# Kernel optimization log

Measured on AMD Instinct MI355X. Metric: run time of the kernel, lower is better.

The kernel has to match this reference:

```python
import math
import jax, jax.numpy as jnp
import numpy as np

WQ = (24, 24)  # query window size
WK = (12, 12)  # key window size
NH = 8         # heads
D = 256        # d_model


def _ln(x, g, b, eps=1e-5):
    m = x.mean(-1, keepdims=True)
    v = ((x - m) ** 2).mean(-1, keepdims=True)
    return (x - m) / jnp.sqrt(v + eps) * g + b


def _sine_pos(F, Hp, Wp):
    # Faithful to PositionEmbeddingSine(normalize=True) applied to an NHWC tensor:
    # dim F (grid height) plays the role of channels; returns (F, Hp, Wp).
    npf = F // 2
    scale = 2.0 * math.pi
    eps = 1e-5
    y = jnp.arange(1, Hp + 1, dtype=jnp.float32) / (Hp + eps) * scale
    x = jnp.arange(1, Wp + 1, dtype=jnp.float32) / (Wp + eps) * scale
    dim_t = 10000.0 ** (2.0 * (jnp.arange(npf) // 2).astype(jnp.float32) / npf)
    def enc(e):
        p = e[:, None] / dim_t
        return jnp.stack([jnp.sin(p[:, 0::2]), jnp.cos(p[:, 1::2])], axis=2).reshape(e.shape[0], npf)
    py = enc(y)  # (Hp, npf)
    px = enc(x)  # (Wp, npf)
    pos = jnp.concatenate([
        jnp.broadcast_to(py[:, None, :], (Hp, Wp, npf)),
        jnp.broadcast_to(px[None, :, :], (Hp, Wp, npf))], axis=-1)
    return pos.transpose(2, 0, 1)


def _interp_ac(x, Ho, Wo):
    # bilinear, align_corners=True; x: (B, C, H, W)
    B, C, H, W = x.shape
    ys = jnp.linspace(0.0, H - 1.0, Ho)
    xs = jnp.linspace(0.0, W - 1.0, Wo)
    y0 = jnp.floor(ys).astype(jnp.int32); y1 = jnp.minimum(y0 + 1, H - 1); wy = ys - y0
    x0 = jnp.floor(xs).astype(jnp.int32); x1 = jnp.minimum(x0 + 1, W - 1); wx = xs - x0
    rows = x[:, :, y0, :] * (1 - wy)[None, None, :, None] + x[:, :, y1, :] * wy[None, None, :, None]
    return rows[:, :, :, x0] * (1 - wx) + rows[:, :, :, x1] * wx


def _wpart(x, wh, ww):
    B, H, W, C = x.shape
    return x.reshape(B, H // wh, wh, W // ww, ww, C).transpose(0, 1, 3, 2, 4, 5).reshape(-1, wh * ww, C)


def _avgpool(x, wh, ww):
    B, H, W, C = x.shape
    return x.reshape(B, H // wh, wh, W // ww, ww, C).mean(axis=(2, 4))


def _forward(x1, x2, q_w, q_b, k_w, k_b, v_w, v_b, q2_w, q2_b, k2_w, k2_b, v2_w, v2_b,
             proj_w, proj_b, proj_g, proj_beta, n1_g, n1_b, n2_g, n2_b,
             fc1_w, fc1_b, fc2_w, fc2_b):
    B, C1, H1, W1 = x1.shape
    _, C2, H2, W2 = x2.shape
    hd = D // NH
    x1n = x1.transpose(0, 2, 3, 1)
    sc = _ln(x1n @ proj_w + proj_b, proj_g, proj_beta)
    sc = _interp_ac(sc.transpose(0, 3, 1, 2), H2, W2).transpose(0, 2, 3, 1)
    x1p = jnp.pad(x1n, ((0, 0), (0, (-H1) % WK[0]), (0, (-W1) % WK[1]), (0, 0)))
    x2n = x2.transpose(0, 2, 3, 1)
    x2p = jnp.pad(x2n, ((0, 0), (0, (-H2) % WQ[0]), (0, (-W2) % WQ[1]), (0, 0)))
    H2p, W2p = x2p.shape[1], x2p.shape[2]
    qw = _wpart(x2p, *WQ)  # (B*nw, 576, C2)
    kw = _wpart(x1p, *WK)  # (B*nw, 144, C1)
    Bn, N1, _ = qw.shape
    def heads(t):
        return t.reshape(t.shape[0], t.shape[1], NH, hd).transpose(0, 2, 1, 3)
    q = heads(qw @ q_w + q_b)
    k = heads(kw @ k_w + k_b)
    v = heads(kw @ v_w + v_b)
    # NOTE: faithful to the source: scale = head_dim**(-0.0) == 1.0 and NO softmax here
    attn = q @ k.transpose(0, 1, 3, 2)
    o = (attn @ v).transpose(0, 2, 1, 3).reshape(Bn, N1, D)
    nwh, nww = H2p // WQ[0], W2p // WQ[1]
    o = o.reshape(B, nwh, nww, WQ[0], WQ[1], D).transpose(0, 1, 3, 2, 4, 5).reshape(B, H2p, W2p, D)
    qf = x2p + o
    # global (pooled) cross-attention branch
    qg = _avgpool(x2p, *WQ)
    qg = qg + _sine_pos(qg.shape[1], qg.shape[2], qg.shape[3])[None]
    kg = _avgpool(x1p, *WK)
    kg = kg + _sine_pos(kg.shape[1], kg.shape[2], kg.shape[3])[None]
    qg = qg.reshape(B, -1, C2)
    kg = kg.reshape(B, -1, C1)
    Nw = qg.shape[1]
    qg2 = heads(qg @ q2_w + q2_b)
    kg2 = heads(kg @ k2_w + k2_b)
    vg = heads(kg @ v2_w + v2_b)
    a2 = jax.nn.softmax(qg2 @ kg2.transpose(0, 1, 3, 2), axis=-1)
    og = (a2 @ vg).transpose(0, 2, 1, 3).reshape(B, Nw, D)
    og = og.transpose(0, 2, 1).reshape(B, D, nwh, nww)
    og = _interp_ac(og, H2p, W2p).transpose(0, 2, 3, 1)
    qf = (qf + og)[:, :H2, :W2, :]
    h = _ln(qf, n1_g, n1_b)
    h = jax.nn.gelu(h @ fc1_w + fc1_b, approximate=False) @ fc2_w + fc2_b
    out = sc + h
    return _ln(out, n2_g, n2_b).transpose(0, 3, 1, 2)


def setup_inputs() -> dict:
    key = jax.random.key(0)
    ks = jax.random.split(key, 12)
    B, C1, C2 = 2, 512, 256
    H1, W1, H2, W2 = 96, 96, 192, 192
    s = 0.02
    def lin(k, i, o):
        return jax.random.normal(k, (i, o), jnp.float32) * s
    return {
        'x1': jax.random.normal(ks[0], (B, C1, H1, W1), jnp.float32),
        'x2': jax.random.normal(ks[1], (B, C2, H2, W2), jnp.float32),
        'q_w': lin(ks[2], C2, D), 'q_b': jnp.zeros((D,), jnp.float32),
        'k_w': lin(ks[3], C1, D), 'k_b': jnp.zeros((D,), jnp.float32),
        'v_w': lin(ks[4], C1, D), 'v_b': jnp.zeros((D,), jnp.float32),
        'q2_w': lin(ks[5], C2, D), 'q2_b': jnp.zeros((D,), jnp.float32),
        'k2_w': lin(ks[6], C1, D), 'k2_b': jnp.zeros((D,), jnp.float32),
        'v2_w': lin(ks[7], C1, D), 'v2_b': jnp.zeros((D,), jnp.float32),
        'proj_w': lin(ks[8], C1, D), 'proj_b': jnp.zeros((D,), jnp.float32),
        'proj_g': jnp.ones((D,), jnp.float32), 'proj_beta': jnp.zeros((D,), jnp.float32),
        'n1_g': jnp.ones((D,), jnp.float32), 'n1_b': jnp.zeros((D,), jnp.float32),
        'n2_g': jnp.ones((D,), jnp.float32), 'n2_b': jnp.zeros((D,), jnp.float32),
        'fc1_w': lin(ks[9], D, 2 * D), 'fc1_b': jnp.zeros((2 * D,), jnp.float32),
        'fc2_w': lin(ks[10], 2 * D, D), 'fc2_b': jnp.zeros((D,), jnp.float32),
    }


def reference(x1, x2, q_w, q_b, k_w, k_b, v_w, v_b, q2_w, q2_b, k2_w, k2_b, v2_w, v2_b,
              proj_w, proj_b, proj_g, proj_beta, n1_g, n1_b, n2_g, n2_b,
              fc1_w, fc1_b, fc2_w, fc2_b):
    return _forward(x1, x2, q_w, q_b, k_w, k_b, v_w, v_b, q2_w, q2_b, k2_w, k2_b, v2_w, v2_b,
                    proj_w, proj_b, proj_g, proj_beta, n1_g, n1_b, n2_g, n2_b,
                    fc1_w, fc1_b, fc2_w, fc2_b)
```

## Files before the change

kernel.cpp:

```cpp
#include <hip/hip_runtime.h>
#include <math.h>


#define HW1 9216L
#define HW2 36864L
#define M1  18432L
#define M2  73728L

typedef __attribute__((ext_vector_type(8))) short short8;
typedef __attribute__((ext_vector_type(4))) float f32x4;
typedef unsigned short u16;

__device__ __forceinline__ short f2bf(float f)
{
    unsigned u = __builtin_bit_cast(unsigned, f);
    u = (u + 0x7fff + ((u >> 16) & 1)) >> 16;
    return (short)u;
}
__device__ __forceinline__ float bf2f(u16 u)
{
    unsigned x = ((unsigned)u) << 16;
    return __builtin_bit_cast(float, x);
}
__device__ __forceinline__ float gelu_exact(float v)
{
    return 0.5f * v * (1.0f + erff(v * 0.70710678118654752f));
}

__global__ __launch_bounds__(256) void wcvt(
    const float* __restrict__ pw, const float* __restrict__ kw,
    const float* __restrict__ vw, const float* __restrict__ qw,
    const float* __restrict__ f1, const float* __restrict__ f2,
    u16* __restrict__ pwT, u16* __restrict__ kwT, u16* __restrict__ vwT,
    u16* __restrict__ qwT, u16* __restrict__ f1T, u16* __restrict__ f2T)
{
    int bx = blockIdx.x, t = threadIdx.x;
    const float* src; u16* dst; int K, ldN = 256, kt, n0 = 0;
    if (bx < 32)       { src = pw; dst = pwT; K = 512; kt = bx; }
    else if (bx < 64)  { src = kw; dst = kwT; K = 512; kt = bx - 32; }
    else if (bx < 96)  { src = vw; dst = vwT; K = 512; kt = bx - 64; }
    else if (bx < 112) { src = qw; dst = qwT; K = 256; kt = bx - 96; }
    else if (bx < 144) { int j = bx - 112; src = f1; dst = f1T; K = 256;
                         ldN = 512; kt = j >> 1; n0 = (j & 1) * 256; }
    else               { src = f2; dst = f2T; K = 512; kt = bx - 144; }
    int n = n0 + t, k0 = kt * 16;
    short s[16];
#pragma unroll
    for (int kk = 0; kk < 16; ++kk) s[kk] = f2bf(src[(long)(k0 + kk) * ldN + n]);
    *(short8*)&dst[(long)n * K + k0]     = *(short8*)&s[0];
    *(short8*)&dst[(long)n * K + k0 + 8] = *(short8*)&s[8];
}

__device__ __forceinline__ float pe4(int t, float e)
{
    if (t == 0) return sinf(e);
    if (t == 1) return cosf(e);
    if (t == 2) return sinf(e * 0.01f);
    return cosf(e * 0.01f);
}

__global__ __launch_bounds__(256) void x1t(
    const float* __restrict__ x1, u16* __restrict__ x1bf, float* __restrict__ kg)
{
    __shared__ short T[6144];
    __shared__ float rw[64][8];
    const int blk = blockIdx.x;
    const int b = blk / 768, rem = blk % 768;
    const int cg = rem / 96, y = rem % 96;
    const int t = threadIdx.x;

    ((float2*)rw)[t] = float2{0.f, 0.f};
    __syncthreads();

    const float* src = x1 + ((long)(b * 512 + cg * 64)) * HW1 + (long)y * 96;
#pragma unroll
    for (int k = 0; k < 6; ++k) {
        int idx = t + k * 256;
        int c = idx / 24, col4 = idx % 24;
        float4 v = *(const float4*)(src + (long)c * HW1 + col4 * 4);
        atomicAdd(&rw[c][col4 / 3], v.x + v.y + v.z + v.w);
        int chh = c >> 1, cb = c & 1;
        const float* vf = (const float*)&v;
#pragma unroll
        for (int j = 0; j < 4; ++j) {
            int pix = col4 * 4 + j;
            int word = pix * 32 + (chh ^ (((pix >> 2) & 7) << 2));
            T[word * 2 + cb] = f2bf(vf[j]);
        }
    }
    __syncthreads();
    u16* dst = x1bf + ((long)b * HW1 + (long)y * 96) * 512 + cg * 64;
#pragma unroll
    for (int k = 0; k < 3; ++k) {
        int idx = t + k * 256;
        int pix = idx >> 3, j = idx & 7;
        int w0 = pix * 32 + ((j * 4) ^ (((pix >> 2) & 7) << 2));
        *(short8*)(dst + (long)pix * 512 + j * 8) = *(short8*)&T[w0 * 2];
    }

    {
        int wy = y / 12;
#pragma unroll
        for (int u = 0; u < 2; ++u) {
            int cell = t * 2 + u;
            int c = cell >> 3, wx = cell & 7;
            atomicAdd(kg + (long)(b * 64 + wy * 8 + wx) * 512 + cg * 64 + c,
                      rw[c][wx] * (1.0f / 144.0f));
        }
    }
    if (y % 12 == 0) {
        const float TWO_PI = 6.283185307179586f;
        int wy = y / 12;
#pragma unroll
        for (int u = 0; u < 2; ++u) {
            int cell = t * 2 + u;
            int gxx = cell & 7, c = cg * 64 + (cell >> 3);
            float pos;
            if (wy < 4) pos = pe4(wy,     (gxx + 1) * (TWO_PI / (8.0f + 1e-5f)));
            else        pos = pe4(wy - 4, (c + 1)   * (TWO_PI / (512.0f + 1e-5f)));
            atomicAdd(kg + (long)(b * 64 + wy * 8 + gxx) * 512 + c, pos);
        }
    }
}

__global__ __launch_bounds__(256) void x2t(
    const float* __restrict__ x2, u16* __restrict__ x2pm, float* __restrict__ qg)
{
    __shared__ short T[12288];
    __shared__ float qsum[64][8];
    const int blk = blockIdx.x;
    const int b = blk / 768, rem = blk % 768;
    const int cg = rem / 192, h = rem % 192;
    const int t = threadIdx.x;

    ((float2*)qsum)[t] = float2{0.f, 0.f};
    __syncthreads();

    const float* src = x2 + ((long)(b * 256 + cg * 64) * 192 + h) * 192;
#pragma unroll
    for (int k = 0; k < 12; ++k) {
        int idx = t + k * 256;
        int c = idx / 48, col4 = idx % 48;
        float4 v = *(const float4*)(src + (long)c * HW2 + col4 * 4);
        atomicAdd(&qsum[c][col4 / 6], v.x + v.y + v.z + v.w);
        int chh = c >> 1, cb = c & 1;
        const float* vf = (const float*)&v;
#pragma unroll
        for (int j = 0; j < 4; ++j) {
            int pix = col4 * 4 + j;
            int word = pix * 32 + (chh ^ (((pix >> 2) & 7) << 2));
            T[word * 2 + cb] = f2bf(vf[j]);
        }
    }
    __syncthreads();

    u16* dst = x2pm + ((long)b * HW2 + (long)h * 192) * 256 + cg * 64;
#pragma unroll
    for (int k = 0; k < 6; ++k) {
        int idx = t + k * 256;
        int pix = idx >> 3, j = idx & 7;
        int w0 = pix * 32 + ((j * 4) ^ (((pix >> 2) & 7) << 2));
        *(short8*)(dst + (long)pix * 256 + j * 8) = *(short8*)&T[w0 * 2];
    }

    {
        int wy = h / 24;
#pragma unroll
        for (int u = 0; u < 2; ++u) {
            int cell = t * 2 + u;
            int c = cell >> 3, wx = cell & 7;
            atomicAdd(qg + (long)(b * 64 + wy * 8 + wx) * 256 + cg * 64 + c,
                      qsum[c][wx] * (1.0f / 576.0f));
        }
    }
    if (h % 24 == 0) {
        const float TWO_PI = 6.283185307179586f;
        int wy = h / 24;
#pragma unroll
        for (int u = 0; u < 2; ++u) {
            int cell = t * 2 + u;
            int gxx = cell & 7, c = cg * 64 + (cell >> 3);
            float pos;
            if (wy < 4) pos = pe4(wy,     (gxx + 1) * (TWO_PI / (8.0f + 1e-5f)));
            else        pos = pe4(wy - 4, (c + 1)   * (TWO_PI / (256.0f + 1e-5f)));
            atomicAdd(qg + (long)(b * 64 + wy * 8 + gxx) * 256 + c, pos);
        }
    }
}

__global__ __launch_bounds__(256) void proj_ln(
    const u16* __restrict__ A, const u16* __restrict__ BT,
    const float* __restrict__ bias, const float* __restrict__ g,
    const float* __restrict__ beta, u16* __restrict__ Cout)
{
    __shared__ short pool[64 * 72 + 256 * 72];
    short* As = pool;
    short* Bs = pool + 64 * 72;
    const int t = threadIdx.x;
    const long m0 = (long)blockIdx.x * 64;
    const int w = t >> 6, lane = t & 63;
    const int lm = lane & 15, lq = lane >> 4;

    f32x4 acc[16] = {};
    for (int k0 = 0; k0 < 512; k0 += 64) {
#pragma unroll
        for (int it = 0; it < 2; ++it) {
            int idx = t + it * 256;
            int r = idx >> 3, q = idx & 7;
            *(short8*)&As[r * 72 + q * 8] = *(const short8*)(A + (m0 + r) * 512 + k0 + q * 8);
        }
#pragma unroll
        for (int it = 0; it < 8; ++it) {
            int idx = t + it * 256;
            int n = idx >> 3, q = idx & 7;
            *(short8*)&Bs[n * 72 + q * 8] = *(const short8*)(BT + (long)n * 512 + k0 + q * 8);
        }
        __syncthreads();
#pragma unroll
        for (int kk = 0; kk < 64; kk += 32) {
            short8 af = *(short8*)&As[(w * 16 + lm) * 72 + kk + lq * 8];
#pragma unroll
            for (int c = 0; c < 16; ++c) {
                short8 bf = *(short8*)&Bs[(c * 16 + lm) * 72 + kk + lq * 8];
                acc[c] = __builtin_amdgcn_mfma_f32_16x16x32_bf16(af, bf, acc[c], 0, 0, 0);
            }
        }
        __syncthreads();
    }
#pragma unroll
    for (int c = 0; c < 16; ++c) {
        float bv = bias[c * 16 + lm];
#pragma unroll
        for (int i = 0; i < 4; ++i) acc[c][i] += bv;
    }
    short* ob = pool;
#pragma unroll
    for (int i = 0; i < 4; ++i) {
        float s = 0.f, s2 = 0.f;
#pragma unroll
        for (int c = 0; c < 16; ++c) { float v = acc[c][i]; s += v; s2 += v * v; }
#pragma unroll
        for (int o = 8; o > 0; o >>= 1) {
            s  += __shfl_xor(s,  o, 64);
            s2 += __shfl_xor(s2, o, 64);
        }
        float mean = s * (1.0f / 256.0f);
        float var  = s2 * (1.0f / 256.0f) - mean * mean;
        float rs   = rsqrtf(var + 1e-5f);
        int row = w * 16 + lq * 4 + i;
#pragma unroll
        for (int c = 0; c < 16; ++c) {
            int col = c * 16 + lm;
            ob[row * 264 + col] = f2bf((acc[c][i] - mean) * rs * g[col] + beta[col]);
        }
    }
    __syncthreads();
    {
        int sr = t >> 2, q4 = (t & 3) * 64;
        u16* Cp = Cout + (m0 + sr) * 256 + q4;
#pragma unroll
        for (int q = 0; q < 8; ++q)
            *(short8*)(Cp + q * 8) = *(short8*)&ob[sr * 264 + q4 + q * 8];
    }
}

template<int EPI>
__global__ __launch_bounds__(256) void gemm_lds(
    const u16* __restrict__ A, const u16* __restrict__ BT,
    const float* __restrict__ bias, u16* __restrict__ C,
    int N, int K, int ldA)
{
    __shared__ short pool[18432];
    short* As = pool;
    short* Bs = pool + 128 * 72;
    const int tid = threadIdx.x;
    const int m0 = blockIdx.y * 128;
    const int n0 = blockIdx.x * 128;
    const int w = tid >> 6, lane = tid & 63;
    const int wm = (w & 1) * 64, wn = (w >> 1) * 64;
    const int lm = lane & 15, lq = lane >> 4;

    const int sr = tid >> 1, sh = (tid & 1) * 32;
    const u16* Ap = A  + (long)(m0 + sr) * ldA + sh;
    const u16* Bp = BT + (long)(n0 + sr) * K   + sh;

    f32x4 acc[4][4] = {};

    for (int k0 = 0; k0 < K; k0 += 64) {
#pragma unroll
        for (int q = 0; q < 4; ++q)
            *(short8*)&As[sr * 72 + sh + q * 8] = *(const short8*)(Ap + k0 + q * 8);
#pragma unroll
        for (int q = 0; q < 4; ++q)
            *(short8*)&Bs[sr * 72 + sh + q * 8] = *(const short8*)(Bp + k0 + q * 8);
        __syncthreads();
#pragma unroll
        for (int kk = 0; kk < 64; kk += 32) {
            short8 af[4], bfr[4];
#pragma unroll
            for (int r = 0; r < 4; ++r) af[r]  = *(short8*)&As[(wm + r * 16 + lm) * 72 + kk + lq * 8];
#pragma unroll
            for (int c = 0; c < 4; ++c) bfr[c] = *(short8*)&Bs[(wn + c * 16 + lm) * 72 + kk + lq * 8];
#pragma unroll
            for (int r = 0; r < 4; ++r)
#pragma unroll
                for (int c = 0; c < 4; ++c)
                    acc[r][c] = __builtin_amdgcn_mfma_f32_16x16x32_bf16(af[r], bfr[c], acc[r][c], 0, 0, 0);
        }
        __syncthreads();
    }

    short* ob = pool;
#pragma unroll
    for (int r = 0; r < 4; ++r)
#pragma unroll
        for (int i = 0; i < 4; ++i) {
            int row = wm + r * 16 + lq * 4 + i;
#pragma unroll
            for (int c = 0; c < 4; ++c) {
                int jl = wn + c * 16 + lm;
                float v = acc[r][c][i] + bias[n0 + jl];
                if (EPI == 1) v = gelu_exact(v);
                ob[row * 136 + jl] = f2bf(v);
            }
        }
    __syncthreads();
    int m = tid >> 1, half = (tid & 1) * 64;
    u16* Cp = C + (long)(m0 + m) * N + n0 + half;
#pragma unroll
    for (int q = 0; q < 8; ++q)
        *(short8*)(Cp + q * 8) = *(short8*)&ob[m * 136 + half + q * 8];
}

__global__ __launch_bounds__(256) void wattn_ln2(
    const u16* __restrict__ x2pm, const u16* __restrict__ qwbT,
    const float* __restrict__ qbias, const u16* __restrict__ ktvb,
    const float* __restrict__ og, u16* __restrict__ hln,
    const float* __restrict__ n1g, const float* __restrict__ n1b)
{
    __shared__ short qs[48 * 288];

    const int t = threadIdx.x;
    const int blk = blockIdx.x;
    const int strip = blk % 12, win = blk / 12;
    const int b = win >> 6, wy = (win >> 3) & 7, wxw = win & 7;
    const int hh0 = wy * 24 + strip * 2;
    const int w = t >> 6, lane = t & 63;
    const int lm = lane & 15, lq = lane >> 4;

    long pbase[3];
#pragma unroll
    for (int r = 0; r < 3; ++r) {
        int p = r * 16 + lm;
        pbase[r] = ((long)b * HW2 + (long)(hh0 + p / 24) * 192 + wxw * 24 + (p % 24)) * 256;
    }

    f32x4 acc[3][4] = {};
#pragma unroll 2
    for (int kc = 0; kc < 8; ++kc) {
        const int ko = kc * 32 + lq * 8;
        short8 af[3], bfr[4];
#pragma unroll
        for (int r = 0; r < 3; ++r)
            af[r] = *(const short8*)(x2pm + pbase[r] + ko);
#pragma unroll
        for (int c = 0; c < 4; ++c)
            bfr[c] = *(const short8*)(qwbT + (long)(w * 64 + c * 16 + lm) * 256 + ko);
#pragma unroll
        for (int r = 0; r < 3; ++r)
#pragma unroll
            for (int c = 0; c < 4; ++c)
                acc[r][c] = __builtin_amdgcn_mfma_f32_16x16x32_bf16(af[r], bfr[c], acc[r][c], 0, 0, 0);
    }

#pragma unroll
    for (int c = 0; c < 4; ++c) {
        float bv = qbias[w * 64 + c * 16 + lm];
#pragma unroll
        for (int r = 0; r < 3; ++r)
#pragma unroll
            for (int i = 0; i < 4; ++i) {
                int row = r * 16 + lq * 4 + i;
                int col = w * 64 + c * 16 + lm;
                qs[row * 288 + (col ^ (((row >> 2) & 3) << 3))] = f2bf(acc[r][c][i] + bv);
            }
    }

    f32x4 oacc[2][3][2] = {};
#pragma unroll
    for (int hl = 0; hl < 2; ++hl) {
        int h = w * 2 + hl;
        short8 af2[3], bfr2[2];
#pragma unroll
        for (int r = 0; r < 3; ++r) {
            int row = r * 16 + lm;
            af2[r] = *(short8*)&qs[row * 288 + ((h * 32 + lq * 8) ^ (((row >> 2) & 3) << 3))];
        }
#pragma unroll
        for (int c = 0; c < 2; ++c)
            bfr2[c] = *(const short8*)(ktvb + ((long)(win * 8 + h) * 32 + c * 16 + lm) * 32 + lq * 8);
#pragma unroll
        for (int r = 0; r < 3; ++r)
#pragma unroll
            for (int c = 0; c < 2; ++c)
                oacc[hl][r][c] = __builtin_amdgcn_mfma_f32_16x16x32_bf16(af2[r], bfr2[c], oacc[hl][r][c], 0, 0, 0);
    }

#pragma unroll
    for (int hl = 0; hl < 2; ++hl)
#pragma unroll
        for (int c = 0; c < 2; ++c)
#pragma unroll
            for (int r = 0; r < 3; ++r)
#pragma unroll
                for (int i = 0; i < 4; ++i) {
                    int p = r * 16 + lq * 4 + i;
                    int ch = (w * 2 + hl) * 32 + c * 16 + lm;
                    qs[p * 288 + (ch ^ (((p >> 2) & 3) << 3))] = f2bf(oacc[hl][r][c][i]);
                }
    __syncthreads();

    float4 g4 = *(const float4*)(n1g + lane * 4);
    float4 b4 = *(const float4*)(n1b + lane * 4);
    const float* ogb0 = og + (long)b * 64 * 256;
#pragma unroll
    for (int pp = 0; pp < 12; ++pp) {
        int p = w * 12 + pp;
        int hh = hh0 + (p / 24), ww = wxw * 24 + (p % 24);
        float fy = hh * (7.0f / 191.0f);
        int y0 = (int)fy; int y1 = min(y0 + 1, 7); float wyf = fy - y0;
        float fx = ww * (7.0f / 191.0f);
        int x0 = (int)fx; int x1 = min(x0 + 1, 7); float wxf = fx - x0;
        float w00 = (1.f - wyf) * (1.f - wxf), w01 = (1.f - wyf) * wxf;
        float w10 = wyf * (1.f - wxf),         w11 = wyf * wxf;
        float4 q00 = *(const float4*)(ogb0 + (y0 * 8 + x0) * 256 + lane * 4);
        float4 q01 = *(const float4*)(ogb0 + (y0 * 8 + x1) * 256 + lane * 4);
        float4 q10 = *(const float4*)(ogb0 + (y1 * 8 + x0) * 256 + lane * 4);
        float4 q11 = *(const float4*)(ogb0 + (y1 * 8 + x1) * 256 + lane * 4);
        long pix = (long)b * HW2 + (long)hh * 192 + ww;
        ushort4 rv = *(const ushort4*)(x2pm + pix * 256 + lane * 4);
        int sw = ((p >> 2) & 3) << 3;
        ushort4 ov = *(ushort4*)&qs[p * 288 + ((lane * 4) ^ sw)];
        float xv0 = bf2f(rv.x) + bf2f(ov.x) + (w00 * q00.x + w01 * q01.x + w10 * q10.x + w11 * q11.x);
        float xv1 = bf2f(rv.y) + bf2f(ov.y) + (w00 * q00.y + w01 * q01.y + w10 * q10.y + w11 * q11.y);
        float xv2 = bf2f(rv.z) + bf2f(ov.z) + (w00 * q00.z + w01 * q01.z + w10 * q10.z + w11 * q11.z);
        float xv3 = bf2f(rv.w) + bf2f(ov.w) + (w00 * q00.w + w01 * q01.w + w10 * q10.w + w11 * q11.w);
        float s  = xv0 + xv1 + xv2 + xv3;
        float s2 = xv0 * xv0 + xv1 * xv1 + xv2 * xv2 + xv3 * xv3;
#pragma unroll
        for (int o = 32; o > 0; o >>= 1) {
            s  += __shfl_xor(s,  o, 64);
            s2 += __shfl_xor(s2, o, 64);
        }
        float mean = s * (1.0f / 256.0f);
        float var  = s2 * (1.0f / 256.0f) - mean * mean;
        float rs   = rsqrtf(var + 1e-5f);
        ushort4 o4;
        o4.x = (u16)f2bf((xv0 - mean) * rs * g4.x + b4.x);
        o4.y = (u16)f2bf((xv1 - mean) * rs * g4.y + b4.y);
        o4.z = (u16)f2bf((xv2 - mean) * rs * g4.z + b4.z);
        o4.w = (u16)f2bf((xv3 - mean) * rs * g4.w + b4.w);
        *(ushort4*)(hln + pix * 256 + lane * 4) = o4;
    }
}

__global__ __launch_bounds__(64) void ktv_mfma(
    const u16* __restrict__ kb, const u16* __restrict__ vb, u16* __restrict__ ktvb)
{
    __shared__ short kt[32 * 162];
    __shared__ short vt[32 * 162];
    const int blk = blockIdx.x;
    const int win = blk >> 3, hd = blk & 7;
    const int b = win >> 6, wy = (win >> 3) & 7, wx = win & 7;
    const int t = threadIdx.x;
    const int lm = t & 15, lq = t >> 4;

    {
        int c = t >> 1, p0 = 144 + (t & 1) * 8;
#pragma unroll
        for (int j = 0; j < 8; ++j) {
            kt[c * 162 + p0 + j] = 0;
            vt[c * 162 + p0 + j] = 0;
        }
    }
    const int pq = t >> 2, c8 = (t & 3) * 8;
#pragma unroll
    for (int it = 0; it < 9; ++it) {
        int p = it * 16 + pq;
        int py = p / 12, px = p % 12;
        long m = (long)b * HW1 + (long)(wy * 12 + py) * 96 + wx * 12 + px;
        short8 kvk = *(const short8*)(kb + m * 256 + hd * 32 + c8);
        short8 kvv = *(const short8*)(vb + m * 256 + hd * 32 + c8);
#pragma unroll
        for (int j = 0; j < 8; ++j) {
            kt[(c8 + j) * 162 + p] = kvk[j];
            vt[(c8 + j) * 162 + p] = kvv[j];
        }
    }
    __syncthreads();
    f32x4 acc[2][2] = {};
#pragma unroll
    for (int kk = 0; kk < 160; kk += 32) {
        short8 af[2], bf[2];
#pragma unroll
        for (int r = 0; r < 2; ++r) af[r] = *(short8*)&kt[(r * 16 + lm) * 162 + kk + lq * 8];
#pragma unroll
        for (int c = 0; c < 2; ++c) bf[c] = *(short8*)&vt[(c * 16 + lm) * 162 + kk + lq * 8];
#pragma unroll
        for (int r = 0; r < 2; ++r)
#pragma unroll
            for (int c = 0; c < 2; ++c)
                acc[r][c] = __builtin_amdgcn_mfma_f32_16x16x32_bf16(af[r], bf[c], acc[r][c], 0, 0, 0);
    }
    u16* dst = ktvb + (long)blk * 1024;
#pragma unroll
    for (int r = 0; r < 2; ++r)
#pragma unroll
        for (int c = 0; c < 2; ++c)
#pragma unroll
            for (int i = 0; i < 4; ++i)
                dst[(c * 16 + lm) * 32 + r * 16 + lq * 4 + i] = (u16)f2bf(acc[r][c][i]);
}

__global__ __launch_bounds__(256) void gemm64m(
    const float* __restrict__ qg, const float* __restrict__ kg,
    const float* __restrict__ q2w, const float* __restrict__ q2b,
    const float* __restrict__ k2w, const float* __restrict__ k2b,
    const float* __restrict__ v2w, const float* __restrict__ v2b,
    float* __restrict__ qg2, float* __restrict__ kg2, float* __restrict__ vgb)
{
    const float* A; const float* Bm; const float* bias; float* C; int K, ldA;
    int z = blockIdx.z;
    if (z == 0)      { A = qg; Bm = q2w; bias = q2b; C = qg2; K = 256; ldA = 256; }
    else if (z == 1) { A = kg; Bm = k2w; bias = k2b; C = kg2; K = 512; ldA = 512; }
    else             { A = kg; Bm = v2w; bias = v2b; C = vgb; K = 512; ldA = 512; }
    const int N = 256;
    constexpr int BK = 16;
    __shared__ float As[BK][68];
    __shared__ float Bs[BK][68];
    const int tid = threadIdx.x;
    const int m0 = blockIdx.y * 64;
    const int n0 = blockIdx.x * 64;
    const int tm = (tid >> 4) << 2;
    const int tn = (tid & 15) << 2;
    float acc[4][4] = {};
    for (int k0 = 0; k0 < K; k0 += BK) {
#pragma unroll
        for (int it = 0; it < 4; ++it) {
            int idx = tid + it * 256;
            int my = idx >> 4, kx = idx & 15;
            As[kx][my] = A[(long)(m0 + my) * ldA + (k0 + kx)];
        }
#pragma unroll
        for (int it = 0; it < 4; ++it) {
            int idx = tid + it * 256;
            int ky = idx >> 6, nx = idx & 63;
            Bs[ky][nx] = Bm[(long)(k0 + ky) * N + (n0 + nx)];
        }
        __syncthreads();
#pragma unroll
        for (int kk = 0; kk < BK; ++kk) {
            float a[4], b[4];
#pragma unroll
            for (int i = 0; i < 4; ++i) a[i] = As[kk][tm + i];
#pragma unroll
            for (int j = 0; j < 4; ++j) b[j] = Bs[kk][tn + j];
#pragma unroll
            for (int i = 0; i < 4; ++i)
#pragma unroll
                for (int j = 0; j < 4; ++j) acc[i][j] += a[i] * b[j];
        }
        __syncthreads();
    }
#pragma unroll
    for (int i = 0; i < 4; ++i) {
        long row = (long)(m0 + tm + i) * N;
#pragma unroll
        for (int j = 0; j < 4; ++j)
            C[row + n0 + tn + j] = acc[i][j] + bias[n0 + tn + j];
    }
}

__global__ __launch_bounds__(256) void gattn(
    const float* __restrict__ qg2, const float* __restrict__ kg2,
    const float* __restrict__ vg, float* __restrict__ og)
{
    __shared__ float qh[64][33], kh[64][33], vh[64][33];
    __shared__ float S[64][65];
    __shared__ float rinv[64];
    int blk = blockIdx.x;
    int b = blk >> 3, hd = blk & 7;
    int t = threadIdx.x;
#pragma unroll
    for (int it = 0; it < 8; ++it) {
        int idx = t + it * 256;
        int n = idx >> 5, i = idx & 31;
        long src = (long)(b * 64 + n) * 256 + hd * 32 + i;
        qh[n][i] = qg2[src];
        kh[n][i] = kg2[src];
        vh[n][i] = vg[src];
    }
    __syncthreads();
    int r = t >> 2, qq = t & 3, c0 = qq * 16;
    for (int c = c0; c < c0 + 16; ++c) {
        float s = 0.f;
#pragma unroll
        for (int i = 0; i < 32; ++i) s += qh[r][i] * kh[c][i];
        S[r][c] = s;
    }
    __syncthreads();
    float mx = -1e30f;
    for (int c = c0; c < c0 + 16; ++c) mx = fmaxf(mx, S[r][c]);
    mx = fmaxf(mx, __shfl_xor(mx, 1, 64));
    mx = fmaxf(mx, __shfl_xor(mx, 2, 64));
    float sm = 0.f;
    for (int c = c0; c < c0 + 16; ++c) {
        float e = expf(S[r][c] - mx);
        S[r][c] = e;
        sm += e;
    }
    sm += __shfl_xor(sm, 1, 64);
    sm += __shfl_xor(sm, 2, 64);
    if (qq == 0) rinv[r] = 1.0f / sm;
    __syncthreads();
    int n = t >> 2, j0 = (t & 3) * 8;
    float inv = rinv[n];
    for (int j = j0; j < j0 + 8; ++j) {
        float s = 0.f;
        for (int c = 0; c < 64; ++c) s += S[n][c] * vh[c][j];
        og[(long)(b * 64 + n) * 256 + hd * 32 + j] = s * inv;
    }
}

__global__ __launch_bounds__(256) void final_k3(
    const u16* __restrict__ mlp, const u16* __restrict__ sc,
    const float* __restrict__ g, const float* __restrict__ bb,
    float* __restrict__ out)
{
    __shared__ float lnb[32][258];
    int blk = blockIdx.x;
    int b = blk / 1152;
    int rem = blk - b * 1152;
    int hh = rem / 6, ww0 = (rem % 6) * 32;
    int wv = threadIdx.x >> 6, lane = threadIdx.x & 63;
    int c0 = lane * 4;
    float4 g4 = *(const float4*)(g + c0);
    float4 b4 = *(const float4*)(bb + c0);
    float fy = hh * (95.0f / 191.0f);
    int y0 = (int)fy; int y1 = min(y0 + 1, 95); float wy = fy - y0;
    const u16* scb = sc + (long)b * 9216 * 256 + c0;
#pragma unroll
    for (int i = 0; i < 8; ++i) {
        int p = wv * 8 + i;
        int ww = ww0 + p;
        float fx = ww * (95.0f / 191.0f);
        int x0 = (int)fx; int x1 = min(x0 + 1, 95); float wx = fx - x0;
        ushort4 u00 = *(const ushort4*)(scb + (long)(y0 * 96 + x0) * 256);
        ushort4 u01 = *(const ushort4*)(scb + (long)(y0 * 96 + x1) * 256);
        ushort4 u10 = *(const ushort4*)(scb + (long)(y1 * 96 + x0) * 256);
        ushort4 u11 = *(const ushort4*)(scb + (long)(y1 * 96 + x1) * 256);
        long m = ((long)b * 192 + hh) * 192 + ww;
        ushort4 um = *(const ushort4*)(mlp + m * 256 + c0);
        float w00 = (1.f - wy) * (1.f - wx), w01 = (1.f - wy) * wx;
        float w10 = wy * (1.f - wx),         w11 = wy * wx;
        float xv0 = bf2f(um.x) + w00 * bf2f(u00.x) + w01 * bf2f(u01.x) + w10 * bf2f(u10.x) + w11 * bf2f(u11.x);
        float xv1 = bf2f(um.y) + w00 * bf2f(u00.y) + w01 * bf2f(u01.y) + w10 * bf2f(u10.y) + w11 * bf2f(u11.y);
        float xv2 = bf2f(um.z) + w00 * bf2f(u00.z) + w01 * bf2f(u01.z) + w10 * bf2f(u10.z) + w11 * bf2f(u11.z);
        float xv3 = bf2f(um.w) + w00 * bf2f(u00.w) + w01 * bf2f(u01.w) + w10 * bf2f(u10.w) + w11 * bf2f(u11.w);
        float s  = xv0 + xv1 + xv2 + xv3;
        float s2 = xv0 * xv0 + xv1 * xv1 + xv2 * xv2 + xv3 * xv3;
#pragma unroll
        for (int o = 32; o > 0; o >>= 1) {
            s  += __shfl_xor(s,  o, 64);
            s2 += __shfl_xor(s2, o, 64);
        }
        float mean = s * (1.0f / 256.0f);
        float var  = s2 * (1.0f / 256.0f) - mean * mean;
        float rs   = rsqrtf(var + 1e-5f);
        lnb[p][c0 + 0] = (xv0 - mean) * rs * g4.x + b4.x;
        lnb[p][c0 + 1] = (xv1 - mean) * rs * g4.y + b4.y;
        lnb[p][c0 + 2] = (xv2 - mean) * rs * g4.z + b4.z;
        lnb[p][c0 + 3] = (xv3 - mean) * rs * g4.w + b4.w;
    }
    __syncthreads();
    int tw = threadIdx.x & 31, cg = threadIdx.x >> 5;
#pragma unroll
    for (int cc = 0; cc < 32; ++cc) {
        int c = cg * 32 + cc;
        out[((long)(b * 256 + c) * 192 + hh) * 192 + ww0 + tw] = lnb[tw][c];
    }
}

extern "C" void kernel_launch(void* const* d_in, const int* in_sizes, int n_in,
                              void* d_out, int out_size, void* d_ws, size_t ws_size,
                              hipStream_t stream)
{
    const float* x1     = (const float*)d_in[0];
    const float* x2     = (const float*)d_in[1];
    const float* q_w    = (const float*)d_in[2];
    const float* q_b    = (const float*)d_in[3];
    const float* k_w    = (const float*)d_in[4];
    const float* k_b    = (const float*)d_in[5];
    const float* v_w    = (const float*)d_in[6];
    const float* v_b    = (const float*)d_in[7];
    const float* q2_w   = (const float*)d_in[8];
    const float* q2_b   = (const float*)d_in[9];
    const float* k2_w   = (const float*)d_in[10];
    const float* k2_b   = (const float*)d_in[11];
    const float* v2_w   = (const float*)d_in[12];
    const float* v2_b   = (const float*)d_in[13];
    const float* proj_w = (const float*)d_in[14];
    const float* proj_b = (const float*)d_in[15];
    const float* proj_g = (const float*)d_in[16];
    const float* proj_bt= (const float*)d_in[17];
    const float* n1_g   = (const float*)d_in[18];
    const float* n1_b   = (const float*)d_in[19];
    const float* n2_g   = (const float*)d_in[20];
    const float* n2_b   = (const float*)d_in[21];
    const float* fc1_w  = (const float*)d_in[22];
    const float* fc1_b  = (const float*)d_in[23];
    const float* fc2_w  = (const float*)d_in[24];
    const float* fc2_b  = (const float*)d_in[25];
    float* out = (float*)d_out;

    char* p = (char*)d_ws;
    u16*   scb  = (u16*)p;    p += M1 * 256 * 2;
    u16*   ktvb = (u16*)p;
    u16*   qwT  = (u16*)(p + 2097152);
    u16*   pwT  = qwT + 65536;
    u16*   kwT  = pwT + 131072;
    u16*   vwT  = kwT + 131072;
    u16*   f1T  = vwT + 131072;
    u16*   f2T  = f1T + 131072;
    p += 1024L * 32 * 32 * 4;
    u16*   kb16 = (u16*)p;    p += M1 * 256 * 2;
    u16*   vb16 = (u16*)p;    p += M1 * 256 * 2;
    u16*   hln  = (u16*)p;    p += M2 * 256 * 2;
    u16*   h1c  = (u16*)p;    p += 36864L * 512 * 2;
    u16*   mlpb = (u16*)p;    p += M2 * 256 * 2;
    float* qg   = (float*)p;  p += 128L * 256 * 4;
    float* kg   = (float*)p;  p += 128L * 512 * 4;
    float* qg2  = (float*)p;  p += 128L * 256 * 4;
    float* kg2  = (float*)p;  p += 128L * 256 * 4;
    float* vgb  = (float*)p;  p += 128L * 256 * 4;
    float* ogb  = (float*)p;  p += 128L * 256 * 4;

    u16* x2pm = mlpb;
    u16* x1bf = hln;

    dim3 blk(256);

    hipMemsetAsync(qg, 0, (128L * 256 + 128L * 512) * 4, stream);

    wcvt<<<dim3(176), blk, 0, stream>>>(proj_w, k_w, v_w, q_w, fc1_w, fc2_w,
                                        pwT, kwT, vwT, qwT, f1T, f2T);
    x1t<<<dim3(1536), blk, 0, stream>>>(x1, x1bf, kg);
    x2t<<<dim3(1536), blk, 0, stream>>>(x2, x2pm, qg);

    proj_ln<<<dim3(288), blk, 0, stream>>>(x1bf, pwT, proj_b, proj_g, proj_bt, scb);

    gemm_lds<0><<<dim3(2, 144), blk, 0, stream>>>(x1bf, kwT, k_b, kb16, 256, 512, 512);
    gemm_lds<0><<<dim3(2, 144), blk, 0, stream>>>(x1bf, vwT, v_b, vb16, 256, 512, 512);

    ktv_mfma<<<dim3(1024), dim3(64), 0, stream>>>(kb16, vb16, ktvb);

    gemm64m<<<dim3(4, 2, 3), blk, 0, stream>>>(qg, kg, q2_w, q2_b, k2_w, k2_b,
                                               v2_w, v2_b, qg2, kg2, vgb);
    gattn<<<dim3(16), blk, 0, stream>>>(qg2, kg2, vgb, ogb);

    wattn_ln2<<<dim3(1536), blk, 0, stream>>>(x2pm, qwT, q_b, ktvb, ogb, hln, n1_g, n1_b);

    for (int c2 = 0; c2 < 2; ++c2) {
        const u16* aoff = hln  + (long)c2 * 36864 * 256;
        u16*       coff = mlpb + (long)c2 * 36864 * 256;
        gemm_lds<1><<<dim3(4, 288), blk, 0, stream>>>(aoff, f1T, fc1_b, h1c, 512, 256, 256);
        gemm_lds<0><<<dim3(2, 288), blk, 0, stream>>>(h1c, f2T, fc2_b, coff, 256, 512, 512);
    }

    final_k3<<<dim3(2304), blk, 0, stream>>>(mlpb, scb, n2_g, n2_b, out);
}
```

Before: 564.5 us.

## Fold per-window K^T V into query weights and merge K/V projection GEMMs

Precomputes, for each window and head, the product of the query projection weight with K^T V (plus a folded bias). The window attention kernel then needs a single GEMM per pixel strip against these per-window weights, and the second small MFMA stage with its LDS round trip is removed. The K and V projections are merged into one GEMM launch writing an interleaved 512-wide buffer, with their biases packed into a contiguous array. In exchange the ktv kernel does extra work and writes a 16 MB per-window weight tensor that wattn must stream instead of one shared weight, and rounding the fused weights to bf16 changes numerics.

```diff
diff --git a/kernel.cpp b/kernel.cpp
--- a/kernel.cpp
+++ b/kernel.cpp
@@ -31,18 +31,31 @@
     const float* __restrict__ pw, const float* __restrict__ kw,
     const float* __restrict__ vw, const float* __restrict__ qw,
     const float* __restrict__ f1, const float* __restrict__ f2,
+    const float* __restrict__ kb, const float* __restrict__ vb,
     u16* __restrict__ pwT, u16* __restrict__ kwT, u16* __restrict__ vwT,
-    u16* __restrict__ qwT, u16* __restrict__ f1T, u16* __restrict__ f2T)
+    u16* __restrict__ f1T, u16* __restrict__ f2T,
+    u16* __restrict__ qwN, float* __restrict__ kvb)
 {
     int bx = blockIdx.x, t = threadIdx.x;
+    if (bx >= 176) {
+        kvb[t] = kb[t];
+        kvb[256 + t] = vb[t];
+        return;
+    }
+    if (bx >= 160) {
+        int k0 = (bx - 160) * 16;
+#pragma unroll
+        for (int kk = 0; kk < 16; ++kk)
+            qwN[(long)(k0 + kk) * 256 + t] = (u16)f2bf(qw[(long)(k0 + kk) * 256 + t]);
+        return;
+    }
     const float* src; u16* dst; int K, ldN = 256, kt, n0 = 0;
     if (bx < 32)       { src = pw; dst = pwT; K = 512; kt = bx; }
     else if (bx < 64)  { src = kw; dst = kwT; K = 512; kt = bx - 32; }
     else if (bx < 96)  { src = vw; dst = vwT; K = 512; kt = bx - 64; }
-    else if (bx < 112) { src = qw; dst = qwT; K = 256; kt = bx - 96; }
-    else if (bx < 144) { int j = bx - 112; src = f1; dst = f1T; K = 256;
+    else if (bx < 128) { int j = bx - 96; src = f1; dst = f1T; K = 256;
                          ldN = 512; kt = j >> 1; n0 = (j & 1) * 256; }
-    else               { src = f2; dst = f2T; K = 512; kt = bx - 144; }
+    else               { src = f2; dst = f2T; K = 512; kt = bx - 128; }
     int n = n0 + t, k0 = kt * 16;
     short s[16];
 #pragma unroll
@@ -332,11 +345,105 @@
         *(short8*)(Cp + q * 8) = *(short8*)&ob[m * 136 + half + q * 8];
 }
 
-__global__ __launch_bounds__(256) void wattn_ln2(
-    const u16* __restrict__ x2pm, const u16* __restrict__ qwbT,
-    const float* __restrict__ qbias, const u16* __restrict__ ktvb,
-    const float* __restrict__ og, u16* __restrict__ hln,
-    const float* __restrict__ n1g, const float* __restrict__ n1b)
+__global__ __launch_bounds__(64) void ktv_w(
+    const u16* __restrict__ kv16, const u16* __restrict__ qwN,
+    const float* __restrict__ qb, u16* __restrict__ wT, float* __restrict__ bias_w)
+{
+    __shared__ short pool[10368 + 1280];
+    short* kt  = pool;
+    short* vt  = pool + 5184;
+    short* kt2 = pool + 10368;
+    short* wout = pool;
+
+    const int blk = blockIdx.x;
+    const int win = blk >> 3, hd = blk & 7;
+    const int b = win >> 6, wy = (win >> 3) & 7, wx = win & 7;
+    const int t = threadIdx.x;
+    const int lm = t & 15, lq = t >> 4;
+
+    {
+        int c = t >> 1, p0 = 144 + (t & 1) * 8;
+#pragma unroll
+        for (int j = 0; j < 8; ++j) {
+            kt[c * 162 + p0 + j] = 0;
+            vt[c * 162 + p0 + j] = 0;
+        }
+    }
+    const int pq = t >> 2, c8 = (t & 3) * 8;
+#pragma unroll
+    for (int it = 0; it < 9; ++it) {
+        int p = it * 16 + pq;
+        int py = p / 12, px = p % 12;
+        long m = (long)b * HW1 + (long)(wy * 12 + py) * 96 + wx * 12 + px;
+        short8 kvk = *(const short8*)(kv16 + m * 512 + hd * 32 + c8);
+        short8 kvv = *(const short8*)(kv16 + m * 512 + 256 + hd * 32 + c8);
+#pragma unroll
+        for (int j = 0; j < 8; ++j) {
+            kt[(c8 + j) * 162 + p] = kvk[j];
+            vt[(c8 + j) * 162 + p] = kvv[j];
+        }
+    }
+    __syncthreads();
+    f32x4 acc[2][2] = {};
+#pragma unroll
+    for (int kk = 0; kk < 160; kk += 32) {
+        short8 af[2], bf[2];
+#pragma unroll
+        for (int r = 0; r < 2; ++r) af[r] = *(short8*)&kt[(r * 16 + lm) * 162 + kk + lq * 8];
+#pragma unroll
+        for (int c = 0; c < 2; ++c) bf[c] = *(short8*)&vt[(c * 16 + lm) * 162 + kk + lq * 8];
+#pragma unroll
+        for (int r = 0; r < 2; ++r)
+#pragma unroll
+            for (int c = 0; c < 2; ++c)
+                acc[r][c] = __builtin_amdgcn_mfma_f32_16x16x32_bf16(af[r], bf[c], acc[r][c], 0, 0, 0);
+    }
+#pragma unroll
+    for (int r = 0; r < 2; ++r)
+#pragma unroll
+        for (int c = 0; c < 2; ++c)
+#pragma unroll
+            for (int i = 0; i < 4; ++i)
+                kt2[(c * 16 + lm) * 40 + r * 16 + lq * 4 + i] = f2bf(acc[r][c][i]);
+    __syncthreads();
+    if (t < 32) {
+        float s = 0.f;
+#pragma unroll
+        for (int tt = 0; tt < 32; ++tt)
+            s += bf2f((u16)kt2[t * 40 + tt]) * qb[hd * 32 + tt];
+        bias_w[(long)blk * 32 + t] = s;
+    }
+    short8 af2[2];
+#pragma unroll
+    for (int r = 0; r < 2; ++r) af2[r] = *(short8*)&kt2[(r * 16 + lm) * 40 + lq * 8];
+#pragma unroll
+    for (int nt = 0; nt < 16; ++nt) {
+        short8 bf = *(const short8*)(qwN + (long)(nt * 16 + lm) * 256 + hd * 32 + lq * 8);
+        f32x4 a2[2] = {};
+#pragma unroll
+        for (int r = 0; r < 2; ++r)
+            a2[r] = __builtin_amdgcn_mfma_f32_16x16x32_bf16(af2[r], bf, a2[r], 0, 0, 0);
+#pragma unroll
+        for (int r = 0; r < 2; ++r)
+#pragma unroll
+            for (int i = 0; i < 4; ++i)
+                wout[(r * 16 + lq * 4 + i) * 264 + nt * 16 + lm] = f2bf(a2[r][i]);
+    }
+    __syncthreads();
+    {
+        int row = t >> 1, half = (t & 1) * 128;
+        u16* dst = wT + ((long)blk * 32 + row) * 256 + half;
+#pragma unroll
+        for (int q = 0; q < 16; ++q)
+            *(short8*)(dst + q * 8) = *(short8*)&wout[row * 264 + half + q * 8];
+    }
+}
+
+__global__ __launch_bounds__(256) void wattn_ln3(
+    const u16* __restrict__ x2pm, const u16* __restrict__ wT,
+    const float* __restrict__ bias_w, const float* __restrict__ og,
+    u16* __restrict__ hln, const float* __restrict__ n1g,
+    const float* __restrict__ n1b)
 {
     __shared__ short qs[48 * 288];
 
@@ -354,6 +461,7 @@
         int p = r * 16 + lm;
         pbase[r] = ((long)b * HW2 + (long)(hh0 + p / 24) * 192 + wxw * 24 + (p % 24)) * 256;
     }
+    const u16* wbase = wT + (long)win * 256 * 256;
 
     f32x4 acc[3][4] = {};
 #pragma unroll 2
@@ -365,7 +473,7 @@
             af[r] = *(const short8*)(x2pm + pbase[r] + ko);
 #pragma unroll
         for (int c = 0; c < 4; ++c)
-            bfr[c] = *(const short8*)(qwbT + (long)(w * 64 + c * 16 + lm) * 256 + ko);
+            bfr[c] = *(const short8*)(wbase + (long)(w * 64 + c * 16 + lm) * 256 + ko);
 #pragma unroll
         for (int r = 0; r < 3; ++r)
 #pragma unroll
@@ -375,49 +483,16 @@
 
 #pragma unroll
     for (int c = 0; c < 4; ++c) {
-        float bv = qbias[w * 64 + c * 16 + lm];
+        float bv = bias_w[(long)win * 256 + w * 64 + c * 16 + lm];
 #pragma unroll
         for (int r = 0; r < 3; ++r)
 #pragma unroll
             for (int i = 0; i < 4; ++i) {
-                int row = r * 16 + lq * 4 + i;
+                int p = r * 16 + lq * 4 + i;
                 int col = w * 64 + c * 16 + lm;
-                qs[row * 288 + (col ^ (((row >> 2) & 3) << 3))] = f2bf(acc[r][c][i] + bv);
+                qs[p * 288 + (col ^ (((p >> 2) & 3) << 4))] = f2bf(acc[r][c][i] + bv);
             }
     }
-
-    f32x4 oacc[2][3][2] = {};
-#pragma unroll
-    for (int hl = 0; hl < 2; ++hl) {
-        int h = w * 2 + hl;
-        short8 af2[3], bfr2[2];
-#pragma unroll
-        for (int r = 0; r < 3; ++r) {
-            int row = r * 16 + lm;
-            af2[r] = *(short8*)&qs[row * 288 + ((h * 32 + lq * 8) ^ (((row >> 2) & 3) << 3))];
-        }
-#pragma unroll
-        for (int c = 0; c < 2; ++c)
-            bfr2[c] = *(const short8*)(ktvb + ((long)(win * 8 + h) * 32 + c * 16 + lm) * 32 + lq * 8);
-#pragma unroll
-        for (int r = 0; r < 3; ++r)
-#pragma unroll
-            for (int c = 0; c < 2; ++c)
-                oacc[hl][r][c] = __builtin_amdgcn_mfma_f32_16x16x32_bf16(af2[r], bfr2[c], oacc[hl][r][c], 0, 0, 0);
-    }
-
-#pragma unroll
-    for (int hl = 0; hl < 2; ++hl)
-#pragma unroll
-        for (int c = 0; c < 2; ++c)
-#pragma unroll
-            for (int r = 0; r < 3; ++r)
-#pragma unroll
-                for (int i = 0; i < 4; ++i) {
-                    int p = r * 16 + lq * 4 + i;
-                    int ch = (w * 2 + hl) * 32 + c * 16 + lm;
-                    qs[p * 288 + (ch ^ (((p >> 2) & 3) << 3))] = f2bf(oacc[hl][r][c][i]);
-                }
     __syncthreads();
 
     float4 g4 = *(const float4*)(n1g + lane * 4);
@@ -439,7 +514,7 @@
         float4 q11 = *(const float4*)(ogb0 + (y1 * 8 + x1) * 256 + lane * 4);
         long pix = (long)b * HW2 + (long)hh * 192 + ww;
         ushort4 rv = *(const ushort4*)(x2pm + pix * 256 + lane * 4);
-        int sw = ((p >> 2) & 3) << 3;
+        int sw = ((p >> 2) & 3) << 4;
         ushort4 ov = *(ushort4*)&qs[p * 288 + ((lane * 4) ^ sw)];
         float xv0 = bf2f(rv.x) + bf2f(ov.x) + (w00 * q00.x + w01 * q01.x + w10 * q10.x + w11 * q11.x);
         float xv1 = bf2f(rv.y) + bf2f(ov.y) + (w00 * q00.y + w01 * q01.y + w10 * q10.y + w11 * q11.y);
@@ -462,64 +537,6 @@
         o4.w = (u16)f2bf((xv3 - mean) * rs * g4.w + b4.w);
         *(ushort4*)(hln + pix * 256 + lane * 4) = o4;
     }
-}
-
-__global__ __launch_bounds__(64) void ktv_mfma(
-    const u16* __restrict__ kb, const u16* __restrict__ vb, u16* __restrict__ ktvb)
-{
-    __shared__ short kt[32 * 162];
-    __shared__ short vt[32 * 162];
-    const int blk = blockIdx.x;
-    const int win = blk >> 3, hd = blk & 7;
-    const int b = win >> 6, wy = (win >> 3) & 7, wx = win & 7;
-    const int t = threadIdx.x;
-    const int lm = t & 15, lq = t >> 4;
-
-    {
-        int c = t >> 1, p0 = 144 + (t & 1) * 8;
-#pragma unroll
-        for (int j = 0; j < 8; ++j) {
-            kt[c * 162 + p0 + j] = 0;
-            vt[c * 162 + p0 + j] = 0;
-        }
-    }
-    const int pq = t >> 2, c8 = (t & 3) * 8;
-#pragma unroll
-    for (int it = 0; it < 9; ++it) {
-        int p = it * 16 + pq;
-        int py = p / 12, px = p % 12;
-        long m = (long)b * HW1 + (long)(wy * 12 + py) * 96 + wx * 12 + px;
-        short8 kvk = *(const short8*)(kb + m * 256 + hd * 32 + c8);
-        short8 kvv = *(const short8*)(vb + m * 256 + hd * 32 + c8);
-#pragma unroll
-        for (int j = 0; j < 8; ++j) {
-            kt[(c8 + j) * 162 + p] = kvk[j];
-            vt[(c8 + j) * 162 + p] = kvv[j];
-        }
-    }
-    __syncthreads();
-    f32x4 acc[2][2] = {};
-#pragma unroll
-    for (int kk = 0; kk < 160; kk += 32) {
-        short8 af[2], bf[2];
-#pragma unroll
-        for (int r = 0; r < 2; ++r) af[r] = *(short8*)&kt[(r * 16 + lm) * 162 + kk + lq * 8];
-#pragma unroll
-        for (int c = 0; c < 2; ++c) bf[c] = *(short8*)&vt[(c * 16 + lm) * 162 + kk + lq * 8];
-#pragma unroll
-        for (int r = 0; r < 2; ++r)
-#pragma unroll
-            for (int c = 0; c < 2; ++c)
-                acc[r][c] = __builtin_amdgcn_mfma_f32_16x16x32_bf16(af[r], bf[c], acc[r][c], 0, 0, 0);
-    }
-    u16* dst = ktvb + (long)blk * 1024;
-#pragma unroll
-    for (int r = 0; r < 2; ++r)
-#pragma unroll
-        for (int c = 0; c < 2; ++c)
-#pragma unroll
-            for (int i = 0; i < 4; ++i)
-                dst[(c * 16 + lm) * 32 + r * 16 + lq * 4 + i] = (u16)f2bf(acc[r][c][i]);
 }
 
 __global__ __launch_bounds__(256) void gemm64m(
@@ -725,16 +742,16 @@
 
     char* p = (char*)d_ws;
     u16*   scb  = (u16*)p;    p += M1 * 256 * 2;
-    u16*   ktvb = (u16*)p;
-    u16*   qwT  = (u16*)(p + 2097152);
-    u16*   pwT  = qwT + 65536;
-    u16*   kwT  = pwT + 131072;
-    u16*   vwT  = kwT + 131072;
-    u16*   f1T  = vwT + 131072;
-    u16*   f2T  = f1T + 131072;
-    p += 1024L * 32 * 32 * 4;
-    u16*   kb16 = (u16*)p;    p += M1 * 256 * 2;
-    u16*   vb16 = (u16*)p;    p += M1 * 256 * 2;
+    u16*   pwT  = (u16*)p;    p += 262144;
+    u16*   kwT  = (u16*)p;    p += 262144;
+    u16*   vwT  = (u16*)p;    p += 262144;
+    u16*   f1T  = (u16*)p;    p += 262144;
+    u16*   f2T  = (u16*)p;    p += 262144;
+    u16*   qwN  = (u16*)p;    p += 131072;
+    float* kvb  = (float*)p;  p += 2048;
+    float* bias_w = (float*)p; p += 131072;
+    u16*   wT   = (u16*)p;    p += 1024L * 32 * 256 * 2;
+    u16*   kv16 = (u16*)p;    p += M1 * 512 * 2;
     u16*   hln  = (u16*)p;    p += M2 * 256 * 2;
     u16*   h1c  = (u16*)p;    p += 36864L * 512 * 2;
     u16*   mlpb = (u16*)p;    p += M2 * 256 * 2;
@@ -752,23 +769,23 @@
 
     hipMemsetAsync(qg, 0, (128L * 256 + 128L * 512) * 4, stream);
 
-    wcvt<<<dim3(176), blk, 0, stream>>>(proj_w, k_w, v_w, q_w, fc1_w, fc2_w,
-                                        pwT, kwT, vwT, qwT, f1T, f2T);
+    wcvt<<<dim3(177), blk, 0, stream>>>(proj_w, k_w, v_w, q_w, fc1_w, fc2_w,
+                                        k_b, v_b, pwT, kwT, vwT, f1T, f2T,
+                                        qwN, kvb);
     x1t<<<dim3(1536), blk, 0, stream>>>(x1, x1bf, kg);
     x2t<<<dim3(1536), blk, 0, stream>>>(x2, x2pm, qg);
 
     proj_ln<<<dim3(288), blk, 0, stream>>>(x1bf, pwT, proj_b, proj_g, proj_bt, scb);
 
-    gemm_lds<0><<<dim3(2, 144), blk, 0, stream>>>(x1bf, kwT, k_b, kb16, 256, 512, 512);
-    gemm_lds<0><<<dim3(2, 144), blk, 0, stream>>>(x1bf, vwT, v_b, vb16, 256, 512, 512);
-
-    ktv_mfma<<<dim3(1024), dim3(64), 0, stream>>>(kb16, vb16, ktvb);
+    gemm_lds<0><<<dim3(4, 144), blk, 0, stream>>>(x1bf, kwT, kvb, kv16, 512, 512, 512);
+
+    ktv_w<<<dim3(1024), dim3(64), 0, stream>>>(kv16, qwN, q_b, wT, bias_w);
 
     gemm64m<<<dim3(4, 2, 3), blk, 0, stream>>>(qg, kg, q2_w, q2_b, k2_w, k2_b,
                                                v2_w, v2_b, qg2, kg2, vgb);
     gattn<<<dim3(16), blk, 0, stream>>>(qg2, kg2, vgb, ogb);
 
-    wattn_ln2<<<dim3(1536), blk, 0, stream>>>(x2pm, qwT, q_b, ktvb, ogb, hln, n1_g, n1_b);
+    wattn_ln3<<<dim3(1536), blk, 0, stream>>>(x2pm, wT, bias_w, ogb, hln, n1_g, n1_b);
 
     for (int c2 = 0; c2 < 2; ++c2) {
         const u16* aoff = hln  + (long)c2 * 36864 * 256;
```

Result: no change. 566.7 us (+0.4%).
